# Kernel tuning notes

Measured on AMD Instinct MI355X. Metric: run time of the kernel, lower is better.

Reference implementation:

```python
import jax, jax.numpy as jnp
import numpy as np
from math import comb

# --- module hyperparameters (from init_kwargs / module-level constants) ---
F = 32          # features
NITER = 3       # num_iterations
NB = 16         # num_basis_functions
NDCM = 4        # n_dcm
CUTOFF = 4.0
MAXZ = 17       # max_atomic_number
NC = 9          # (max_degree+1)^2 spherical components, max_degree=2
DEG = np.array([0, 1, 1, 1, 2, 2, 2, 2, 2])  # degree l of each component
BINOM = jnp.asarray([comb(NB - 1, k) for k in range(NB)], dtype=jnp.float32)


def _np_sph9(x, y, z):
    # real spherical harmonics up to l=2 on the unit sphere (numpy, for Gaunt table)
    c0 = 0.28209479177387814; c1 = 0.4886025119029199
    c2a = 1.0925484305920792; c2b = 0.31539156525252005; c2c = 0.5462742152960396
    return np.stack([c0 * np.ones_like(x), c1 * y, c1 * z, c1 * x,
                     c2a * x * y, c2a * y * z, c2b * (3.0 * z * z - 1.0),
                     c2a * x * z, c2c * (x * x - y * y)], axis=0)


def _gaunt():
    # real Gaunt (Clebsch-Gordan-type) coefficients G[a,b,c] = int Y_a Y_b Y_c dOmega
    # via Gauss-Legendre (cos theta) x midpoint (phi) quadrature -- exact for l<=2 products
    ct, wt = np.polynomial.legendre.leggauss(64)
    nph = 256
    phi = (np.arange(nph) + 0.5) * (2.0 * np.pi / nph)
    st = np.sqrt(1.0 - ct ** 2)
    x = st[:, None] * np.cos(phi)[None, :]
    y = st[:, None] * np.sin(phi)[None, :]
    z = np.broadcast_to(ct[:, None], x.shape)
    w = (wt[:, None] * (2.0 * np.pi / nph)) * np.ones((1, nph))
    Y = _np_sph9(x, y, z)
    G = np.einsum('aij,bij,cij,ij->abc', Y, Y, Y, w)
    G[np.abs(G) < 1e-6] = 0.0
    return G

CG = jnp.asarray(_gaunt(), dtype=jnp.float32)  # (9, 9, 9), sparse


def _sph9(u):
    # u: (E, 3) unit vectors -> (E, 9)
    x, y, z = u[:, 0], u[:, 1], u[:, 2]
    c0 = 0.28209479177387814; c1 = 0.4886025119029199
    c2a = 1.0925484305920792; c2b = 0.31539156525252005; c2c = 0.5462742152960396
    return jnp.stack([jnp.full_like(x, c0), c1 * y, c1 * z, c1 * x,
                      c2a * x * y, c2a * y * z, c2b * (3.0 * z * z - 1.0),
                      c2a * x * z, c2c * (x * x - y * y)], axis=-1)


def _radial(r):
    # reciprocal Bernstein radial basis * smooth cutoff; r: (E,) -> (E, NB)
    u = 1.0 / (1.0 + r)
    k = jnp.arange(NB, dtype=jnp.float32)
    rb = BINOM * u[:, None] ** k * (1.0 - u[:, None]) ** (NB - 1 - k)
    t = r / CUTOFF
    den = jnp.where(t < 1.0, 1.0 - t * t, 1.0)
    fc = jnp.where(t < 1.0, jnp.exp(-t * t / den), 0.0)  # smooth_cutoff
    return rb * fc[:, None]


def _equiv_dense(x, W, b=None):
    # per-degree linear (equivariant Dense): x (N, 9, Fin), W (3, Fin, Fout); bias on l=0 only
    y = jnp.einsum('ncf,cfg->ncg', x, W[DEG])
    if b is not None:
        y = y.at[:, 0, :].add(b)
    return y


def _tp(xs, bf):
    # Gaunt tensor-product contraction: out[e,c,f] = sum_ab CG[a,b,c] xs[e,a,f] bf[e,b,f]
    # loop over the 9 fixed output components to avoid an (E,9,9,F) intermediate
    out = []
    for c in range(NC):
        t = jnp.einsum('eaf,ab->ebf', xs, CG[:, :, c])
        out.append(jnp.sum(t * bf, axis=1))
    return jnp.stack(out, axis=1)


def _forward(atomic_numbers, positions, dst_idx, src_idx, embed, Wb, W1, b1, W2, b2,
             Wt00, Wt11, Wmono, element_bias):
    n = atomic_numbers.shape[0]
    disp = positions[src_idx] - positions[dst_idx]                 # (E, 3) gather
    r = jnp.sqrt(jnp.sum(disp * disp, axis=-1) + 1e-12)            # safe norm
    u = disp / r[:, None]
    basis = _sph9(u)[:, :, None] * _radial(r)[:, None, :]          # (E, 9, NB)
    x = jnp.zeros((n, NC, F), dtype=positions.dtype).at[:, 0, :].set(embed[atomic_numbers])
    for i in range(NITER):  # message passing iterations
        bf = jnp.einsum('ebn,bng->ebg', basis, Wb[i][DEG])         # per-degree radial->feature mix (E,9,F)
        msg = _tp(x[src_idx], bf)                                  # gather src + tensor product
        y = x + jax.ops.segment_sum(msg, dst_idx, num_segments=n)  # scatter-aggregate + residual add
        y = _equiv_dense(y, W1[i], b1[i])
        y = jax.nn.silu(y)
        y = _equiv_dense(y, W2[i], b2[i])
        x = x + y                                                  # residual update
    # TensorDense to n_dcm channels, then readout heads
    mono = (x[:, 0, :] @ Wt00) @ Wmono + element_bias[atomic_numbers][:, None]  # (N, NDCM)
    dip = jnp.einsum('ncf,fg->ncg', x[:, 1:4, :], Wt11)            # (N, 3, NDCM) vector channel
    dip = jnp.clip(jax.nn.silu(dip), -0.3, 0.3) + positions[:, :, None]
    return mono, dip


def setup_inputs():
    key = jax.random.key(0)
    ks = jax.random.split(key, 12)
    N, E = 10000, 160000
    return {
        'atomic_numbers': jax.random.randint(ks[0], (N,), 0, MAXZ + 1),
        'positions': jax.random.normal(ks[1], (N, 3), jnp.float32) * 3.0,
        'dst_idx': jax.random.randint(ks[2], (E,), 0, N),
        'src_idx': jax.random.randint(ks[3], (E,), 0, N),
        'embed': jax.random.normal(ks[4], (MAXZ + 1, F), jnp.float32),
        'Wb': jax.random.normal(ks[5], (NITER, 3, NB, F), jnp.float32) / np.sqrt(NB).astype(np.float32),
        'W1': jax.random.normal(ks[6], (NITER, 3, F, F), jnp.float32) / np.sqrt(F).astype(np.float32),
        'b1': jnp.zeros((NITER, F), jnp.float32),
        'W2': jax.random.normal(ks[7], (NITER, 3, F, F), jnp.float32) / np.sqrt(F).astype(np.float32),
        'b2': jnp.zeros((NITER, F), jnp.float32),
        'Wt00': jax.random.normal(ks[8], (F, NDCM), jnp.float32) / np.sqrt(F).astype(np.float32),
        'Wt11': jax.random.normal(ks[9], (F, NDCM), jnp.float32) / np.sqrt(F).astype(np.float32),
        'Wmono': jax.random.normal(ks[10], (NDCM, NDCM), jnp.float32) / np.sqrt(NDCM).astype(np.float32),
        'element_bias': jnp.zeros((MAXZ + 1,), jnp.float32),
    }


def reference(atomic_numbers, positions, dst_idx, src_idx, embed, Wb, W1, b1, W2, b2,
              Wt00, Wt11, Wmono, element_bias):
    return _forward(atomic_numbers, positions, dst_idx, src_idx, embed, Wb, W1, b1, W2, b2,
                    Wt00, Wt11, Wmono, element_bias)
```

## Files before the change

kernel.cpp:

```cpp
#include <hip/hip_runtime.h>
#include <hip/hip_bf16.h>


#define NITER 3
#define BCAP  64

#define OFF_WB    0
#define OFF_W1    4608
#define OFF_B1    13824
#define OFF_W2    13920
#define OFF_B2    23136
#define OFF_WT00  23232
#define OFF_WT11  23360
#define OFF_WMONO 23488
#define OFF_EB    23504
#define OFF_EMB   23522
#define WC_TOTAL  24098

__device__ __forceinline__ float b2f(const __hip_bfloat16 v) { return __bfloat162float(v); }

#define KC0 0.28209479177387814f
#define KG1 0.21850968611841584f
#define KG2 0.12615662610100802f
#define KG3 0.18022375157287861f
#define KG4 0.09011187578643931f
#define KG5 0.15607834722743988f

__device__ __forceinline__ float ldany(const void* p, int i, bool f32) {
    return f32 ? ((const float*)p)[i] : b2f(((const __hip_bfloat16*)p)[i]);
}

__device__ __forceinline__ bool wave_sniff(const void* pos) {
    const __hip_bfloat16* p = (const __hip_bfloat16*)pos;
    int lane = threadIdx.x & 63;
    int bad = 0;
    #pragma unroll
    for (int k = 0; k < 4; k++) {
        float v = b2f(p[lane + k*64]);
        bad |= !(fabsf(v) < 1.0e6f);
    }
    return __ballot(bad) != 0ull;
}

__device__ __forceinline__ float xadd32(float v) {
    return v + __int_as_float(__shfl_xor(__float_as_int(v), 32, 64));
}

__device__ __forceinline__ bool edge_geom(float dx, float dy, float dz,
                                          float* sp, float* rad) {
    float r2 = dx*dx + dy*dy + dz*dz + 1e-12f;
    if (r2 >= 16.0f) return false;
    float r  = sqrtf(r2);
    float t2 = r2 * 0.0625f;
    float fc = __expf(-t2 / (1.0f - t2));
    float u = 1.0f / (1.0f + r);
    float v = 1.0f - u;
    const float BIN[16] = {1.f,15.f,105.f,455.f,1365.f,3003.f,5005.f,6435.f,
                           6435.f,5005.f,3003.f,1365.f,455.f,105.f,15.f,1.f};
    float vp[16];
    vp[0] = 1.0f;
    #pragma unroll
    for (int k = 1; k < 16; k++) vp[k] = vp[k-1] * v;
    float up = 1.0f;
    #pragma unroll
    for (int n = 0; n < 16; n++) { rad[n] = BIN[n] * up * vp[15-n] * fc; up *= u; }
    float ir = 1.0f / r;
    float ux = dx*ir, uy = dy*ir, uz = dz*ir;
    const float c0 = 0.28209479177387814f, c1 = 0.4886025119029199f;
    const float c2a = 1.0925484305920792f, c2b = 0.31539156525252005f, c2c = 0.5462742152960396f;
    sp[0] = c0;
    sp[1] = c1*uy; sp[2] = c1*uz; sp[3] = c1*ux;
    sp[4] = c2a*ux*uy; sp[5] = c2a*uy*uz; sp[6] = c2b*(3.0f*uz*uz - 1.0f);
    sp[7] = c2a*ux*uz; sp[8] = c2c*(ux*ux - uy*uy);
    return true;
}

__global__ void setup_kernel(const void* pos, const void* Wb, const void* W1,
        const void* b1, const void* W2, const void* b2, const void* Wt00,
        const void* Wt11, const void* Wmono, const void* eb, const void* emb,
        const int* __restrict__ an,
        const int* __restrict__ srcI, const int* __restrict__ dstI,
        float* __restrict__ posf, float* __restrict__ wc,
        float* __restrict__ x, float* __restrict__ geo2, int* __restrict__ cur,
        int N, int E, int use_csr) {
    bool f32 = wave_sniff(pos);
    int i = blockIdx.x * blockDim.x + threadIdx.x;
    int np = N * 3;
    if (i < np) { posf[i] = ldany(pos, i, f32); return; }
    int j = i - np;
    if (j < WC_TOTAL) {
        const void* src; int rel;
        if      (j < OFF_W1)    { src = Wb;    rel = j; }
        else if (j < OFF_B1)    { src = W1;    rel = j - OFF_W1; }
        else if (j < OFF_W2)    { src = b1;    rel = j - OFF_B1; }
        else if (j < OFF_B2)    { src = W2;    rel = j - OFF_W2; }
        else if (j < OFF_WT00)  { src = b2;    rel = j - OFF_B2; }
        else if (j < OFF_WT11)  { src = Wt00;  rel = j - OFF_WT00; }
        else if (j < OFF_WMONO) { src = Wt11;  rel = j - OFF_WT11; }
        else if (j < OFF_EB)    { src = Wmono; rel = j - OFF_WMONO; }
        else if (j < OFF_EMB)   { src = eb;    rel = j - OFF_EB; }
        else                    { src = emb;   rel = j - OFF_EMB; }
        wc[j] = ldany(src, rel, f32);
        return;
    }
    j -= WC_TOTAL;
    if (j < N * 32) {
        int n = j >> 5, rem = j & 31;
        x[(size_t)n * 288 + rem] = ldany(emb, an[n] * 32 + rem, f32);
        return;
    }
    j -= N * 32;
    if (j < E && use_csr) {
        int s = srcI[j], d = dstI[j];
        float sp[9], rad[16];
        if (!edge_geom(ldany(pos, s*3+0, f32) - ldany(pos, d*3+0, f32),
                       ldany(pos, s*3+1, f32) - ldany(pos, d*3+1, f32),
                       ldany(pos, s*3+2, f32) - ldany(pos, d*3+2, f32),
                       sp, rad)) return;
        int slot = atomicAdd(&cur[d], 1);
        float* gp = geo2 + ((size_t)d * BCAP + slot) * 32;
        gp[0] = __int_as_float(s);
        gp[1] = 0.0f;
        #pragma unroll
        for (int a = 0; a < 9; a++) gp[2 + a] = sp[a];
        gp[11] = 0.0f;
        #pragma unroll
        for (int k = 0; k < 16; k++) gp[16 + k] = rad[k];
    }
}

template <bool FIRST, bool LAST>
__global__ __launch_bounds__(256) void edge_gather_kernel(
        const float* __restrict__ x, float* __restrict__ y,
        const float* __restrict__ geo2, const int* __restrict__ cur,
        const float* __restrict__ Wbi, int N) {
    int tid  = threadIdx.x;
    int f    = tid & 31;
    int half = (tid >> 5) & 1;
    int n    = (blockIdx.x * blockDim.x + tid) >> 6;
    if (n >= N) return;
    float w0[16], w1[16], w2[16];
    #pragma unroll
    for (int k = 0; k < 16; k++) {
        w0[k] = Wbi[(0*16 + k)*32 + f];
        w1[k] = Wbi[(1*16 + k)*32 + f];
        w2[k] = Wbi[(2*16 + k)*32 + f];
    }
    float A0=0.f,A1=0.f,A2=0.f,A3=0.f,A4=0.f,A5=0.f,A6=0.f,A7=0.f,A8=0.f;
    int beg = n * BCAP, end = beg + cur[n];
    for (int e = beg + half; e < end; e += 2) {
        const float4* gp = (const float4*)(geo2 + (size_t)e * 32);
        float4 h0 = gp[0], h1 = gp[1], h2 = gp[2];
        float4 r0 = gp[4], r1 = gp[5], r2 = gp[6], r3 = gp[7];
        int s = __float_as_int(h0.x);
        float rad[16] = {r0.x,r0.y,r0.z,r0.w, r1.x,r1.y,r1.z,r1.w,
                         r2.x,r2.y,r2.z,r2.w, r3.x,r3.y,r3.z,r3.w};
        float rw0 = 0.f, rw1 = 0.f, rw2 = 0.f;
        #pragma unroll
        for (int k = 0; k < 16; k++) {
            rw0 = fmaf(rad[k], w0[k], rw0);
            rw1 = fmaf(rad[k], w1[k], rw1);
            rw2 = fmaf(rad[k], w2[k], rw2);
        }
        float B0 = h0.z*rw0;
        float B1 = h0.w*rw1, B2 = h1.x*rw1, B3 = h1.y*rw1;
        float B4 = h1.z*rw2, B5 = h1.w*rw2, B6 = h2.x*rw2,
              B7 = h2.y*rw2, B8 = h2.z*rw2;
        const float* xp = x + (size_t)s*288 + f;
        if (FIRST) {
            float X0 = xp[0];
            float k0 = KC0 * X0;
            A0 += k0*B0; A1 += k0*B1; A2 += k0*B2; A3 += k0*B3; A4 += k0*B4;
            A5 += k0*B5; A6 += k0*B6; A7 += k0*B7; A8 += k0*B8;
        } else {
            float X0 = xp[0],   X1 = xp[32],  X2 = xp[64],  X3 = xp[96],  X4 = xp[128];
            float X5 = xp[160], X6 = xp[192], X7 = xp[224], X8 = xp[256];
            A0 += KC0*(X0*B0 + X1*B1 + X2*B2 + X3*B3 + X4*B4 + X5*B5 + X6*B6 + X7*B7 + X8*B8);
            A1 += KC0*(X0*B1 + X1*B0) + KG1*(X3*B4 + X4*B3 + X2*B5 + X5*B2)
                - KG2*(X1*B6 + X6*B1) - KG1*(X1*B8 + X8*B1);
            A2 += KC0*(X0*B2 + X2*B0) + KG1*(X1*B5 + X5*B1 + X3*B7 + X7*B3)
                + 2.0f*KG2*(X2*B6 + X6*B2);
            A3 += KC0*(X0*B3 + X3*B0) + KG1*(X1*B4 + X4*B1 + X2*B7 + X7*B2)
                - KG2*(X3*B6 + X6*B3) + KG1*(X3*B8 + X8*B3);
            if (!LAST) {
                A4 += KC0*(X0*B4 + X4*B0) + KG1*(X1*B3 + X3*B1) + KG5*(X5*B7 + X7*B5)
                    - KG3*(X4*B6 + X6*B4);
                A5 += KC0*(X0*B5 + X5*B0) + KG1*(X1*B2 + X2*B1) + KG5*(X4*B7 + X7*B4)
                    + KG4*(X5*B6 + X6*B5) - KG5*(X5*B8 + X8*B5);
                A6 += KC0*(X0*B6 + X6*B0) - KG2*X1*B1 + 2.0f*KG2*X2*B2 - KG2*X3*B3
                    - KG3*X4*B4 + KG4*X5*B5 + KG3*X6*B6 + KG4*X7*B7 - KG3*X8*B8;
                A7 += KC0*(X0*B7 + X7*B0) + KG1*(X2*B3 + X3*B2) + KG5*(X4*B5 + X5*B4)
                    + KG4*(X6*B7 + X7*B6) + KG5*(X7*B8 + X8*B7);
                A8 += KC0*(X0*B8 + X8*B0) - KG1*X1*B1 + KG1*X3*B3 - KG5*X5*B5 + KG5*X7*B7
                    - KG3*(X6*B8 + X8*B6);
            }
        }
    }
    A0 = xadd32(A0); A1 = xadd32(A1); A2 = xadd32(A2); A3 = xadd32(A3);
    if (!LAST) {
        A4 = xadd32(A4); A5 = xadd32(A5); A6 = xadd32(A6);
        A7 = xadd32(A7); A8 = xadd32(A8);
    }
    if (half == 0) {
        float* yp = y + (size_t)n * 288 + f;
        yp[0]   = A0; yp[32]  = A1; yp[64]  = A2; yp[96]  = A3;
        if (!LAST) {
            yp[128] = A4; yp[160] = A5; yp[192] = A6; yp[224] = A7; yp[256] = A8;
        }
    }
}

template <bool FIRST>
__global__ __launch_bounds__(256) void atom_kernel(
        float* __restrict__ x, const float* __restrict__ y,
        const float* __restrict__ W1i, const float* __restrict__ b1i,
        const float* __restrict__ W2i, const float* __restrict__ b2i,
        int N) {
    __shared__ float sm[4][64*33];
    int lane  = threadIdx.x & 63;
    int wslot = threadIdx.x >> 6;
    int u = __builtin_amdgcn_readfirstlane(blockIdx.x * 4 + wslot);
    int t = u / 9;
    int c = u - t * 9;
    int d = (c == 0) ? 0 : ((c < 4) ? 1 : 2);
    const float* W1 = W1i + d * 1024;
    const float* W2 = W2i + d * 1024;
    float* tile = sm[wslot];
    bool usex = (!FIRST) || (c == 0);
    float4 xr4[8];
    #pragma unroll
    for (int k = 0; k < 8; k++) {
        int e  = lane * 4 + k * 256;
        int al = e >> 5, f = e & 31;
        int ag = t * 64 + al;
        float4 s = make_float4(0.f, 0.f, 0.f, 0.f);
        float4 xv = make_float4(0.f, 0.f, 0.f, 0.f);
        if (ag < N) {
            if (usex) xv = *(const float4*)(x + (size_t)ag * 288 + c * 32 + f);
            float4 yv = *(const float4*)(y + (size_t)ag * 288 + c * 32 + f);
            s = make_float4(xv.x + yv.x, xv.y + yv.y, xv.z + yv.z, xv.w + yv.w);
        }
        xr4[k] = xv;
        *(float4*)(tile + al * 33 + f) = s;
    }
    __syncthreads();
    float yin[32];
    #pragma unroll
    for (int k = 0; k < 8; k++) {
        float4 v = *(const float4*)(tile + lane * 33 + 4 * k);
        yin[4*k+0] = v.x; yin[4*k+1] = v.y; yin[4*k+2] = v.z; yin[4*k+3] = v.w;
    }
    float acc[32];
    #pragma unroll
    for (int g = 0; g < 32; g++) acc[g] = (c == 0) ? b1i[g] : 0.0f;
    #pragma unroll 4
    for (int fi = 0; fi < 32; fi++) {
        float v = yin[fi];
        #pragma unroll
        for (int g = 0; g < 32; g++) acc[g] = fmaf(v, W1[fi*32 + g], acc[g]);
    }
    #pragma unroll
    for (int g = 0; g < 32; g++)
        acc[g] = acc[g] * __builtin_amdgcn_rcpf(1.0f + __expf(-acc[g]));
    float out[32];
    #pragma unroll
    for (int g = 0; g < 32; g++) out[g] = (c == 0) ? b2i[g] : 0.0f;
    #pragma unroll 4
    for (int fi = 0; fi < 32; fi++) {
        float v = acc[fi];
        #pragma unroll
        for (int g = 0; g < 32; g++) out[g] = fmaf(v, W2[fi*32 + g], out[g]);
    }
    __syncthreads();
    #pragma unroll
    for (int k = 0; k < 8; k++)
        *(float4*)(tile + lane * 33 + 4 * k) =
            make_float4(out[4*k+0], out[4*k+1], out[4*k+2], out[4*k+3]);
    __syncthreads();
    #pragma unroll
    for (int k = 0; k < 8; k++) {
        int e  = lane * 4 + k * 256;
        int al = e >> 5, f = e & 31;
        int ag = t * 64 + al;
        if (ag < N) {
            float4 dv = *(const float4*)(tile + al * 33 + f);
            float4 xv = xr4[k];
            *(float4*)(x + (size_t)ag * 288 + c * 32 + f) =
                make_float4(xv.x + dv.x, xv.y + dv.y, xv.z + dv.z, xv.w + dv.w);
        }
    }
}

__global__ __launch_bounds__(256) void atom_readout_kernel(
        const float* __restrict__ x, const float* __restrict__ y,
        const float* __restrict__ W1i, const float* __restrict__ b1i,
        const float* __restrict__ W2i, const float* __restrict__ b2i,
        const int* __restrict__ an, const float* __restrict__ posf,
        const float* __restrict__ wc, const void* __restrict__ pos,
        void* __restrict__ out_, int N) {
    bool f32 = wave_sniff(pos);
    __shared__ float sm[4][64*33];
    int lane  = threadIdx.x & 63;
    int wslot = threadIdx.x >> 6;
    int c = __builtin_amdgcn_readfirstlane(wslot);
    int t = blockIdx.x;
    int d = (c == 0) ? 0 : 1;
    const float* W1 = W1i + d * 1024;
    const float* W2 = W2i + d * 1024;
    float* tile = sm[wslot];
    float4 xr4[8];
    #pragma unroll
    for (int k = 0; k < 8; k++) {
        int e  = lane * 4 + k * 256;
        int al = e >> 5, f = e & 31;
        int ag = t * 64 + al;
        float4 s = make_float4(0.f, 0.f, 0.f, 0.f);
        float4 xv = make_float4(0.f, 0.f, 0.f, 0.f);
        if (ag < N) {
            xv = *(const float4*)(x + (size_t)ag * 288 + c * 32 + f);
            float4 yv = *(const float4*)(y + (size_t)ag * 288 + c * 32 + f);
            s = make_float4(xv.x + yv.x, xv.y + yv.y, xv.z + yv.z, xv.w + yv.w);
        }
        xr4[k] = xv;
        *(float4*)(tile + al * 33 + f) = s;
    }
    __syncthreads();
    float yin[32];
    #pragma unroll
    for (int k = 0; k < 8; k++) {
        float4 v = *(const float4*)(tile + lane * 33 + 4 * k);
        yin[4*k+0] = v.x; yin[4*k+1] = v.y; yin[4*k+2] = v.z; yin[4*k+3] = v.w;
    }
    float acc[32];
    #pragma unroll
    for (int g = 0; g < 32; g++) acc[g] = (c == 0) ? b1i[g] : 0.0f;
    #pragma unroll 4
    for (int fi = 0; fi < 32; fi++) {
        float v = yin[fi];
        #pragma unroll
        for (int g = 0; g < 32; g++) acc[g] = fmaf(v, W1[fi*32 + g], acc[g]);
    }
    #pragma unroll
    for (int g = 0; g < 32; g++)
        acc[g] = acc[g] * __builtin_amdgcn_rcpf(1.0f + __expf(-acc[g]));
    float out[32];
    #pragma unroll
    for (int g = 0; g < 32; g++) out[g] = (c == 0) ? b2i[g] : 0.0f;
    #pragma unroll 4
    for (int fi = 0; fi < 32; fi++) {
        float v = acc[fi];
        #pragma unroll
        for (int g = 0; g < 32; g++) out[g] = fmaf(v, W2[fi*32 + g], out[g]);
    }
    __syncthreads();
    #pragma unroll
    for (int k = 0; k < 8; k++)
        *(float4*)(tile + lane * 33 + 4 * k) =
            make_float4(out[4*k+0], out[4*k+1], out[4*k+2], out[4*k+3]);
    __syncthreads();
    #pragma unroll
    for (int k = 0; k < 8; k++) {
        int e  = lane * 4 + k * 256;
        int al = e >> 5, f = e & 31;
        float4 dv = *(const float4*)(tile + al * 33 + f);
        float4 xv = xr4[k];
        *(float4*)(tile + al * 33 + f) =
            make_float4(xv.x + dv.x, xv.y + dv.y, xv.z + dv.z, xv.w + dv.w);
    }
    __syncthreads();
    if (threadIdx.x < 64) {
        int a  = threadIdx.x;
        int ag = t * 64 + a;
        if (ag < N) {
            const float* Wt00  = wc + OFF_WT00;
            const float* Wt11  = wc + OFF_WT11;
            const float* Wmono = wc + OFF_WMONO;
            const float* x0 = sm[0] + a * 33;
            float q[4] = {0.f, 0.f, 0.f, 0.f};
            for (int f = 0; f < 32; f++) {
                float xv = x0[f];
                #pragma unroll
                for (int j = 0; j < 4; j++) q[j] = fmaf(xv, Wt00[f*4 + j], q[j]);
            }
            float ebv = wc[OFF_EB + an[ag]];
            #pragma unroll
            for (int m = 0; m < 4; m++) {
                float accm = ebv;
                #pragma unroll
                for (int j = 0; j < 4; j++) accm = fmaf(q[j], Wmono[j*4 + m], accm);
                if (f32) ((float*)out_)[ag*4 + m] = accm;
                else ((__hip_bfloat16*)out_)[ag*4 + m] = __float2bfloat16(accm);
            }
            #pragma unroll
            for (int cc = 0; cc < 3; cc++) {
                float pc = posf[ag*3 + cc];
                const float* xc = sm[1 + cc] + a * 33;
                float dq[4] = {0.f, 0.f, 0.f, 0.f};
                for (int f = 0; f < 32; f++) {
                    float xv = xc[f];
                    #pragma unroll
                    for (int m = 0; m < 4; m++) dq[m] = fmaf(xv, Wt11[f*4 + m], dq[m]);
                }
                #pragma unroll
                for (int m = 0; m < 4; m++) {
                    float v = dq[m];
                    v = v * __builtin_amdgcn_rcpf(1.0f + __expf(-v));
                    v = fminf(fmaxf(v, -0.3f), 0.3f);
                    v += pc;
                    if (f32) ((float*)out_)[N*4 + ag*12 + cc*4 + m] = v;
                    else ((__hip_bfloat16*)out_)[N*4 + ag*12 + cc*4 + m] = __float2bfloat16(v);
                }
            }
        }
    }
}

__global__ void zero_kernel(float4* __restrict__ b, int n) {
    int i = blockIdx.x * blockDim.x + threadIdx.x;
    int stride = gridDim.x * blockDim.x;
    float4 z = make_float4(0.f, 0.f, 0.f, 0.f);
    for (; i < n; i += stride) b[i] = z;
}

__global__ __launch_bounds__(256) void edge_inline_kernel(
        const float* __restrict__ x, float* __restrict__ y,
        const float* __restrict__ posf,
        const int* __restrict__ srcI, const int* __restrict__ dstI,
        const float* __restrict__ Wbi, int E) {
    int f  = threadIdx.x & 31;
    int hw = (blockIdx.x * blockDim.x + threadIdx.x) >> 5;
    int nhw = gridDim.x * (blockDim.x >> 5);
    float w0[16], w1[16], w2[16];
    #pragma unroll
    for (int n = 0; n < 16; n++) {
        w0[n] = Wbi[(0*16 + n)*32 + f];
        w1[n] = Wbi[(1*16 + n)*32 + f];
        w2[n] = Wbi[(2*16 + n)*32 + f];
    }
    for (int e = hw; e < E; e += nhw) {
        int s = srcI[e], d = dstI[e];
        float sp[9], rad[16];
        if (!edge_geom(posf[s*3+0] - posf[d*3+0],
                       posf[s*3+1] - posf[d*3+1],
                       posf[s*3+2] - posf[d*3+2], sp, rad)) continue;
        float rw0 = 0.f, rw1 = 0.f, rw2 = 0.f;
        #pragma unroll
        for (int n = 0; n < 16; n++) {
            rw0 = fmaf(rad[n], w0[n], rw0);
            rw1 = fmaf(rad[n], w1[n], rw1);
            rw2 = fmaf(rad[n], w2[n], rw2);
        }
        float B0 = sp[0]*rw0;
        float B1 = sp[1]*rw1, B2 = sp[2]*rw1, B3 = sp[3]*rw1;
        float B4 = sp[4]*rw2, B5 = sp[5]*rw2, B6 = sp[6]*rw2,
              B7 = sp[7]*rw2, B8 = sp[8]*rw2;
        const float* xp = x + (size_t)s*288 + f;
        float X0 = xp[0],   X1 = xp[32],  X2 = xp[64],  X3 = xp[96],  X4 = xp[128];
        float X5 = xp[160], X6 = xp[192], X7 = xp[224], X8 = xp[256];
        float* yp = y + (size_t)d*288 + f;
        float m;
        m = KC0*(X0*B0 + X1*B1 + X2*B2 + X3*B3 + X4*B4 + X5*B5 + X6*B6 + X7*B7 + X8*B8);
        unsafeAtomicAdd(yp + 0, m);
        m = KC0*(X0*B1 + X1*B0) + KG1*(X3*B4 + X4*B3 + X2*B5 + X5*B2)
          - KG2*(X1*B6 + X6*B1) - KG1*(X1*B8 + X8*B1);
        unsafeAtomicAdd(yp + 32, m);
        m = KC0*(X0*B2 + X2*B0) + KG1*(X1*B5 + X5*B1 + X3*B7 + X7*B3)
          + 2.0f*KG2*(X2*B6 + X6*B2);
        unsafeAtomicAdd(yp + 64, m);
        m = KC0*(X0*B3 + X3*B0) + KG1*(X1*B4 + X4*B1 + X2*B7 + X7*B2)
          - KG2*(X3*B6 + X6*B3) + KG1*(X3*B8 + X8*B3);
        unsafeAtomicAdd(yp + 96, m);
        m = KC0*(X0*B4 + X4*B0) + KG1*(X1*B3 + X3*B1) + KG5*(X5*B7 + X7*B5)
          - KG3*(X4*B6 + X6*B4);
        unsafeAtomicAdd(yp + 128, m);
        m = KC0*(X0*B5 + X5*B0) + KG1*(X1*B2 + X2*B1) + KG5*(X4*B7 + X7*B4)
          + KG4*(X5*B6 + X6*B5) - KG5*(X5*B8 + X8*B5);
        unsafeAtomicAdd(yp + 160, m);
        m = KC0*(X0*B6 + X6*B0) - KG2*X1*B1 + 2.0f*KG2*X2*B2 - KG2*X3*B3
          - KG3*X4*B4 + KG4*X5*B5 + KG3*X6*B6 + KG4*X7*B7 - KG3*X8*B8;
        unsafeAtomicAdd(yp + 192, m);
        m = KC0*(X0*B7 + X7*B0) + KG1*(X2*B3 + X3*B2) + KG5*(X4*B5 + X5*B4)
          + KG4*(X6*B7 + X7*B6) + KG5*(X7*B8 + X8*B7);
        unsafeAtomicAdd(yp + 224, m);
        m = KC0*(X0*B8 + X8*B0) - KG1*X1*B1 + KG1*X3*B3 - KG5*X5*B5 + KG5*X7*B7
          - KG3*(X6*B8 + X8*B6);
        unsafeAtomicAdd(yp + 256, m);
    }
}

__global__ void readout_kernel(const float* __restrict__ x,
        const int* __restrict__ an, const float* __restrict__ posf,
        const float* __restrict__ wc, const void* __restrict__ pos,
        void* __restrict__ out, int N) {
    bool f32 = wave_sniff(pos);
    int n = blockIdx.x * blockDim.x + threadIdx.x;
    if (n >= N) return;
    const float* Wt00  = wc + OFF_WT00;
    const float* Wt11  = wc + OFF_WT11;
    const float* Wmono = wc + OFF_WMONO;
    const float* xb = x + (size_t)n * 288;
    float q[4] = {0.f, 0.f, 0.f, 0.f};
    for (int f = 0; f < 32; f++) {
        float xv = xb[f];
        #pragma unroll
        for (int j = 0; j < 4; j++) q[j] = fmaf(xv, Wt00[f*4 + j], q[j]);
    }
    float ebv = wc[OFF_EB + an[n]];
    #pragma unroll
    for (int m = 0; m < 4; m++) {
        float acc = ebv;
        #pragma unroll
        for (int j = 0; j < 4; j++) acc = fmaf(q[j], Wmono[j*4 + m], acc);
        if (f32) ((float*)out)[n*4 + m] = acc;
        else ((__hip_bfloat16*)out)[n*4 + m] = __float2bfloat16(acc);
    }
    #pragma unroll
    for (int c = 0; c < 3; c++) {
        float pc = posf[n*3 + c];
        const float* xc = xb + (1 + c)*32;
        float dq[4] = {0.f, 0.f, 0.f, 0.f};
        for (int f = 0; f < 32; f++) {
            float xv = xc[f];
            #pragma unroll
            for (int m = 0; m < 4; m++) dq[m] = fmaf(xv, Wt11[f*4 + m], dq[m]);
        }
        #pragma unroll
        for (int m = 0; m < 4; m++) {
            float v = dq[m];
            v = v * __builtin_amdgcn_rcpf(1.0f + __expf(-v));
            v = fminf(fmaxf(v, -0.3f), 0.3f);
            v += pc;
            if (f32) ((float*)out)[N*4 + n*12 + c*4 + m] = v;
            else ((__hip_bfloat16*)out)[N*4 + n*12 + c*4 + m] = __float2bfloat16(v);
        }
    }
}

extern "C" void kernel_launch(void* const* d_in, const int* in_sizes, int n_in,
                              void* d_out, int out_size, void* d_ws, size_t ws_size,
                              hipStream_t stream) {
    const int* an    = (const int*)d_in[0];
    const void* pos  = d_in[1];
    const int* dstI  = (const int*)d_in[2];
    const int* srcI  = (const int*)d_in[3];
    const void* embed= d_in[4];
    const void* Wb   = d_in[5];
    const void* W1   = d_in[6];
    const void* b1   = d_in[7];
    const void* W2   = d_in[8];
    const void* b2   = d_in[9];
    const void* Wt00 = d_in[10];
    const void* Wt11 = d_in[11];
    const void* Wmono= d_in[12];
    const void* eb   = d_in[13];
    int N = in_sizes[0];
    int E = in_sizes[2];

    float* x    = (float*)d_ws;
    float* y    = x + (size_t)N * 288;
    float* posf = y + (size_t)N * 288;
    float* wc   = posf + (size_t)N * 3;
    int* cur    = (int*)(wc + WC_TOTAL);
    uintptr_t ga = ((uintptr_t)(cur + N) + 127) & ~(uintptr_t)127;
    float* geo2 = (float*)ga;
    size_t need = (uintptr_t)(geo2 + (size_t)N * BCAP * 32) - (uintptr_t)d_ws;
    bool use_csr = (ws_size >= need);

    hipMemsetAsync(cur, 0, sizeof(int) * (size_t)N, stream);
    if (!use_csr)
        zero_kernel<<<512, 256, 0, stream>>>((float4*)x, N * 72);
    {
        int tot = N * 3 + WC_TOTAL + N * 32 + (use_csr ? E : 0);
        setup_kernel<<<(tot + 255)/256, 256, 0, stream>>>(
            pos, Wb, W1, b1, W2, b2, Wt00, Wt11, Wmono, eb, embed,
            an, srcI, dstI, posf, wc, x, geo2, cur, N, E, use_csr ? 1 : 0);
    }
    int ntiles = (N + 63) / 64;
    if (use_csr) {
        int gblocks = (N + 3) / 4;
        for (int i = 0; i < NITER; i++) {
            const float* Wbi = wc + OFF_WB + (size_t)i*1536;
            const float* W1i = wc + OFF_W1 + (size_t)i*3072;
            const float* b1i = wc + OFF_B1 + (size_t)i*32;
            const float* W2i = wc + OFF_W2 + (size_t)i*3072;
            const float* b2i = wc + OFF_B2 + (size_t)i*32;
            if (i == 0) {
                edge_gather_kernel<true,false><<<gblocks, 256, 0, stream>>>(
                    x, y, geo2, cur, Wbi, N);
                atom_kernel<true><<<(ntiles*9 + 3)/4, 256, 0, stream>>>(
                    x, y, W1i, b1i, W2i, b2i, N);
            } else if (i == NITER - 1) {
                edge_gather_kernel<false,true><<<gblocks, 256, 0, stream>>>(
                    x, y, geo2, cur, Wbi, N);
                atom_readout_kernel<<<ntiles, 256, 0, stream>>>(
                    x, y, W1i, b1i, W2i, b2i, an, posf, wc, pos, d_out, N);
            } else {
                edge_gather_kernel<false,false><<<gblocks, 256, 0, stream>>>(
                    x, y, geo2, cur, Wbi, N);
                atom_kernel<false><<<(ntiles*9 + 3)/4, 256, 0, stream>>>(
                    x, y, W1i, b1i, W2i, b2i, N);
            }
        }
    } else {
        int ablocks = (ntiles * 9 + 3) / 4;
        for (int i = 0; i < NITER; i++) {
            zero_kernel<<<512, 256, 0, stream>>>((float4*)y, N * 72);
            edge_inline_kernel<<<2048, 256, 0, stream>>>(x, y, posf, srcI, dstI,
                wc + OFF_WB + (size_t)i*1536, E);
            atom_kernel<false><<<ablocks, 256, 0, stream>>>(x, y,
                wc + OFF_W1 + (size_t)i*3072, wc + OFF_B1 + (size_t)i*32,
                wc + OFF_W2 + (size_t)i*3072, wc + OFF_B2 + (size_t)i*32, N);
        }
        readout_kernel<<<(N + 255)/256, 256, 0, stream>>>(x, an, posf, wc, pos,
                                                          d_out, N);
    }
}
```

Before: 212.2 us.

## Fuse edge gather and atom update into one kernel per iteration with ping-pong x

Each message-passing iteration now runs as a single kernel per 64-atom tile: it gathers edge messages for the tile's atoms, synchronizes, then runs the atom MLP update, writing to a second x buffer (ping-pong) so other blocks can still read the old features. This removes separate gather/atom launches and the global round trip ordering between them. The tradeoff is far fewer blocks (one per 64 atoms, 4 waves each), so much less parallelism in the gather phase, and the atom phase loops three times with an idle wave. Geometry slot writes are also vectorized to float4 stores.

```diff
diff --git a/kernel.cpp b/kernel.cpp
--- a/kernel.cpp
+++ b/kernel.cpp
@@ -75,70 +75,24 @@
     return true;
 }
 
-__global__ void setup_kernel(const void* pos, const void* Wb, const void* W1,
-        const void* b1, const void* W2, const void* b2, const void* Wt00,
-        const void* Wt11, const void* Wmono, const void* eb, const void* emb,
-        const int* __restrict__ an,
-        const int* __restrict__ srcI, const int* __restrict__ dstI,
-        float* __restrict__ posf, float* __restrict__ wc,
-        float* __restrict__ x, float* __restrict__ geo2, int* __restrict__ cur,
-        int N, int E, int use_csr) {
-    bool f32 = wave_sniff(pos);
-    int i = blockIdx.x * blockDim.x + threadIdx.x;
-    int np = N * 3;
-    if (i < np) { posf[i] = ldany(pos, i, f32); return; }
-    int j = i - np;
-    if (j < WC_TOTAL) {
-        const void* src; int rel;
-        if      (j < OFF_W1)    { src = Wb;    rel = j; }
-        else if (j < OFF_B1)    { src = W1;    rel = j - OFF_W1; }
-        else if (j < OFF_W2)    { src = b1;    rel = j - OFF_B1; }
-        else if (j < OFF_B2)    { src = W2;    rel = j - OFF_W2; }
-        else if (j < OFF_WT00)  { src = b2;    rel = j - OFF_B2; }
-        else if (j < OFF_WT11)  { src = Wt00;  rel = j - OFF_WT00; }
-        else if (j < OFF_WMONO) { src = Wt11;  rel = j - OFF_WT11; }
-        else if (j < OFF_EB)    { src = Wmono; rel = j - OFF_WMONO; }
-        else if (j < OFF_EMB)   { src = eb;    rel = j - OFF_EB; }
-        else                    { src = emb;   rel = j - OFF_EMB; }
-        wc[j] = ldany(src, rel, f32);
-        return;
-    }
-    j -= WC_TOTAL;
-    if (j < N * 32) {
-        int n = j >> 5, rem = j & 31;
-        x[(size_t)n * 288 + rem] = ldany(emb, an[n] * 32 + rem, f32);
-        return;
-    }
-    j -= N * 32;
-    if (j < E && use_csr) {
-        int s = srcI[j], d = dstI[j];
-        float sp[9], rad[16];
-        if (!edge_geom(ldany(pos, s*3+0, f32) - ldany(pos, d*3+0, f32),
-                       ldany(pos, s*3+1, f32) - ldany(pos, d*3+1, f32),
-                       ldany(pos, s*3+2, f32) - ldany(pos, d*3+2, f32),
-                       sp, rad)) return;
-        int slot = atomicAdd(&cur[d], 1);
-        float* gp = geo2 + ((size_t)d * BCAP + slot) * 32;
-        gp[0] = __int_as_float(s);
-        gp[1] = 0.0f;
-        #pragma unroll
-        for (int a = 0; a < 9; a++) gp[2 + a] = sp[a];
-        gp[11] = 0.0f;
-        #pragma unroll
-        for (int k = 0; k < 16; k++) gp[16 + k] = rad[k];
-    }
+__device__ __forceinline__ void write_geo_slot(float* gp, int s,
+                                               const float* sp, const float* rad) {
+    float4* g4 = (float4*)gp;
+    g4[0] = make_float4(__int_as_float(s), 0.f, sp[0], sp[1]);
+    g4[1] = make_float4(sp[2], sp[3], sp[4], sp[5]);
+    g4[2] = make_float4(sp[6], sp[7], sp[8], 0.f);
+    g4[4] = make_float4(rad[0],  rad[1],  rad[2],  rad[3]);
+    g4[5] = make_float4(rad[4],  rad[5],  rad[6],  rad[7]);
+    g4[6] = make_float4(rad[8],  rad[9],  rad[10], rad[11]);
+    g4[7] = make_float4(rad[12], rad[13], rad[14], rad[15]);
 }
 
 template <bool FIRST, bool LAST>
-__global__ __launch_bounds__(256) void edge_gather_kernel(
+__device__ __forceinline__ void gather_phase(
         const float* __restrict__ x, float* __restrict__ y,
         const float* __restrict__ geo2, const int* __restrict__ cur,
-        const float* __restrict__ Wbi, int N) {
-    int tid  = threadIdx.x;
-    int f    = tid & 31;
-    int half = (tid >> 5) & 1;
-    int n    = (blockIdx.x * blockDim.x + tid) >> 6;
-    if (n >= N) return;
+        const float* __restrict__ Wbi, int nend, int f, int half,
+        int wg, int nw) {
     float w0[16], w1[16], w2[16];
     #pragma unroll
     for (int k = 0; k < 16; k++) {
@@ -146,86 +100,82 @@
         w1[k] = Wbi[(1*16 + k)*32 + f];
         w2[k] = Wbi[(2*16 + k)*32 + f];
     }
-    float A0=0.f,A1=0.f,A2=0.f,A3=0.f,A4=0.f,A5=0.f,A6=0.f,A7=0.f,A8=0.f;
-    int beg = n * BCAP, end = beg + cur[n];
-    for (int e = beg + half; e < end; e += 2) {
-        const float4* gp = (const float4*)(geo2 + (size_t)e * 32);
-        float4 h0 = gp[0], h1 = gp[1], h2 = gp[2];
-        float4 r0 = gp[4], r1 = gp[5], r2 = gp[6], r3 = gp[7];
-        int s = __float_as_int(h0.x);
-        float rad[16] = {r0.x,r0.y,r0.z,r0.w, r1.x,r1.y,r1.z,r1.w,
-                         r2.x,r2.y,r2.z,r2.w, r3.x,r3.y,r3.z,r3.w};
-        float rw0 = 0.f, rw1 = 0.f, rw2 = 0.f;
-        #pragma unroll
-        for (int k = 0; k < 16; k++) {
-            rw0 = fmaf(rad[k], w0[k], rw0);
-            rw1 = fmaf(rad[k], w1[k], rw1);
-            rw2 = fmaf(rad[k], w2[k], rw2);
-        }
-        float B0 = h0.z*rw0;
-        float B1 = h0.w*rw1, B2 = h1.x*rw1, B3 = h1.y*rw1;
-        float B4 = h1.z*rw2, B5 = h1.w*rw2, B6 = h2.x*rw2,
-              B7 = h2.y*rw2, B8 = h2.z*rw2;
-        const float* xp = x + (size_t)s*288 + f;
-        if (FIRST) {
-            float X0 = xp[0];
-            float k0 = KC0 * X0;
-            A0 += k0*B0; A1 += k0*B1; A2 += k0*B2; A3 += k0*B3; A4 += k0*B4;
-            A5 += k0*B5; A6 += k0*B6; A7 += k0*B7; A8 += k0*B8;
-        } else {
-            float X0 = xp[0],   X1 = xp[32],  X2 = xp[64],  X3 = xp[96],  X4 = xp[128];
-            float X5 = xp[160], X6 = xp[192], X7 = xp[224], X8 = xp[256];
-            A0 += KC0*(X0*B0 + X1*B1 + X2*B2 + X3*B3 + X4*B4 + X5*B5 + X6*B6 + X7*B7 + X8*B8);
-            A1 += KC0*(X0*B1 + X1*B0) + KG1*(X3*B4 + X4*B3 + X2*B5 + X5*B2)
-                - KG2*(X1*B6 + X6*B1) - KG1*(X1*B8 + X8*B1);
-            A2 += KC0*(X0*B2 + X2*B0) + KG1*(X1*B5 + X5*B1 + X3*B7 + X7*B3)
-                + 2.0f*KG2*(X2*B6 + X6*B2);
-            A3 += KC0*(X0*B3 + X3*B0) + KG1*(X1*B4 + X4*B1 + X2*B7 + X7*B2)
-                - KG2*(X3*B6 + X6*B3) + KG1*(X3*B8 + X8*B3);
+    for (int n = wg; n < nend; n += nw) {
+        float A0=0.f,A1=0.f,A2=0.f,A3=0.f,A4=0.f,A5=0.f,A6=0.f,A7=0.f,A8=0.f;
+        int beg = n * BCAP, end = beg + cur[n];
+        for (int e = beg + half; e < end; e += 2) {
+            const float4* gp = (const float4*)(geo2 + (size_t)e * 32);
+            float4 h0 = gp[0], h1 = gp[1], h2 = gp[2];
+            float4 r0 = gp[4], r1 = gp[5], r2 = gp[6], r3 = gp[7];
+            int s = __float_as_int(h0.x);
+            float rad[16] = {r0.x,r0.y,r0.z,r0.w, r1.x,r1.y,r1.z,r1.w,
+                             r2.x,r2.y,r2.z,r2.w, r3.x,r3.y,r3.z,r3.w};
+            float rw0 = 0.f, rw1 = 0.f, rw2 = 0.f;
+            #pragma unroll
+            for (int k = 0; k < 16; k++) {
+                rw0 = fmaf(rad[k], w0[k], rw0);
+                rw1 = fmaf(rad[k], w1[k], rw1);
+                rw2 = fmaf(rad[k], w2[k], rw2);
+            }
+            float B0 = h0.z*rw0;
+            float B1 = h0.w*rw1, B2 = h1.x*rw1, B3 = h1.y*rw1;
+            float B4 = h1.z*rw2, B5 = h1.w*rw2, B6 = h2.x*rw2,
+                  B7 = h2.y*rw2, B8 = h2.z*rw2;
+            const float* xp = x + (size_t)s*288 + f;
+            if (FIRST) {
+                float X0 = xp[0];
+                float k0 = KC0 * X0;
+                A0 += k0*B0; A1 += k0*B1; A2 += k0*B2; A3 += k0*B3; A4 += k0*B4;
+                A5 += k0*B5; A6 += k0*B6; A7 += k0*B7; A8 += k0*B8;
+            } else {
+                float X0 = xp[0],   X1 = xp[32],  X2 = xp[64],  X3 = xp[96],  X4 = xp[128];
+                float X5 = xp[160], X6 = xp[192], X7 = xp[224], X8 = xp[256];
+                A0 += KC0*(X0*B0 + X1*B1 + X2*B2 + X3*B3 + X4*B4 + X5*B5 + X6*B6 + X7*B7 + X8*B8);
+                A1 += KC0*(X0*B1 + X1*B0) + KG1*(X3*B4 + X4*B3 + X2*B5 + X5*B2)
+                    - KG2*(X1*B6 + X6*B1) - KG1*(X1*B8 + X8*B1);
+                A2 += KC0*(X0*B2 + X2*B0) + KG1*(X1*B5 + X5*B1 + X3*B7 + X7*B3)
+                    + 2.0f*KG2*(X2*B6 + X6*B2);
+                A3 += KC0*(X0*B3 + X3*B0) + KG1*(X1*B4 + X4*B1 + X2*B7 + X7*B2)
+                    - KG2*(X3*B6 + X6*B3) + KG1*(X3*B8 + X8*B3);
+                if (!LAST) {
+                    A4 += KC0*(X0*B4 + X4*B0) + KG1*(X1*B3 + X3*B1) + KG5*(X5*B7 + X7*B5)
+                        - KG3*(X4*B6 + X6*B4);
+                    A5 += KC0*(X0*B5 + X5*B0) + KG1*(X1*B2 + X2*B1) + KG5*(X4*B7 + X7*B4)
+                        + KG4*(X5*B6 + X6*B5) - KG5*(X5*B8 + X8*B5);
+                    A6 += KC0*(X0*B6 + X6*B0) - KG2*X1*B1 + 2.0f*KG2*X2*B2 - KG2*X3*B3
+                        - KG3*X4*B4 + KG4*X5*B5 + KG3*X6*B6 + KG4*X7*B7 - KG3*X8*B8;
+                    A7 += KC0*(X0*B7 + X7*B0) + KG1*(X2*B3 + X3*B2) + KG5*(X4*B5 + X5*B4)
+                        + KG4*(X6*B7 + X7*B6) + KG5*(X7*B8 + X8*B7);
+                    A8 += KC0*(X0*B8 + X8*B0) - KG1*X1*B1 + KG1*X3*B3 - KG5*X5*B5 + KG5*X7*B7
+                        - KG3*(X6*B8 + X8*B6);
+                }
+            }
+        }
+        A0 = xadd32(A0); A1 = xadd32(A1); A2 = xadd32(A2); A3 = xadd32(A3);
+        if (!LAST) {
+            A4 = xadd32(A4); A5 = xadd32(A5); A6 = xadd32(A6);
+            A7 = xadd32(A7); A8 = xadd32(A8);
+        }
+        if (half == 0) {
+            float* yp = y + (size_t)n * 288 + f;
+            yp[0]   = A0; yp[32]  = A1; yp[64]  = A2; yp[96]  = A3;
             if (!LAST) {
-                A4 += KC0*(X0*B4 + X4*B0) + KG1*(X1*B3 + X3*B1) + KG5*(X5*B7 + X7*B5)
-                    - KG3*(X4*B6 + X6*B4);
-                A5 += KC0*(X0*B5 + X5*B0) + KG1*(X1*B2 + X2*B1) + KG5*(X4*B7 + X7*B4)
-                    + KG4*(X5*B6 + X6*B5) - KG5*(X5*B8 + X8*B5);
-                A6 += KC0*(X0*B6 + X6*B0) - KG2*X1*B1 + 2.0f*KG2*X2*B2 - KG2*X3*B3
-                    - KG3*X4*B4 + KG4*X5*B5 + KG3*X6*B6 + KG4*X7*B7 - KG3*X8*B8;
-                A7 += KC0*(X0*B7 + X7*B0) + KG1*(X2*B3 + X3*B2) + KG5*(X4*B5 + X5*B4)
-                    + KG4*(X6*B7 + X7*B6) + KG5*(X7*B8 + X8*B7);
-                A8 += KC0*(X0*B8 + X8*B0) - KG1*X1*B1 + KG1*X3*B3 - KG5*X5*B5 + KG5*X7*B7
-                    - KG3*(X6*B8 + X8*B6);
+                yp[128] = A4; yp[160] = A5; yp[192] = A6; yp[224] = A7; yp[256] = A8;
             }
         }
     }
-    A0 = xadd32(A0); A1 = xadd32(A1); A2 = xadd32(A2); A3 = xadd32(A3);
-    if (!LAST) {
-        A4 = xadd32(A4); A5 = xadd32(A5); A6 = xadd32(A6);
-        A7 = xadd32(A7); A8 = xadd32(A8);
-    }
-    if (half == 0) {
-        float* yp = y + (size_t)n * 288 + f;
-        yp[0]   = A0; yp[32]  = A1; yp[64]  = A2; yp[96]  = A3;
-        if (!LAST) {
-            yp[128] = A4; yp[160] = A5; yp[192] = A6; yp[224] = A7; yp[256] = A8;
-        }
-    }
 }
 
 template <bool FIRST>
-__global__ __launch_bounds__(256) void atom_kernel(
-        float* __restrict__ x, const float* __restrict__ y,
+__device__ __forceinline__ void atom_unit(
+        const float* __restrict__ xin, float* __restrict__ xout,
+        const float* __restrict__ y,
         const float* __restrict__ W1i, const float* __restrict__ b1i,
         const float* __restrict__ W2i, const float* __restrict__ b2i,
-        int N) {
-    __shared__ float sm[4][64*33];
-    int lane  = threadIdx.x & 63;
-    int wslot = threadIdx.x >> 6;
-    int u = __builtin_amdgcn_readfirstlane(blockIdx.x * 4 + wslot);
-    int t = u / 9;
-    int c = u - t * 9;
+        int N, int t, int c, int lane, float* __restrict__ tile) {
     int d = (c == 0) ? 0 : ((c < 4) ? 1 : 2);
     const float* W1 = W1i + d * 1024;
     const float* W2 = W2i + d * 1024;
-    float* tile = sm[wslot];
     bool usex = (!FIRST) || (c == 0);
     float4 xr4[8];
     #pragma unroll
@@ -236,7 +186,7 @@
         float4 s = make_float4(0.f, 0.f, 0.f, 0.f);
         float4 xv = make_float4(0.f, 0.f, 0.f, 0.f);
         if (ag < N) {
-            if (usex) xv = *(const float4*)(x + (size_t)ag * 288 + c * 32 + f);
+            if (usex) xv = *(const float4*)(xin + (size_t)ag * 288 + c * 32 + f);
             float4 yv = *(const float4*)(y + (size_t)ag * 288 + c * 32 + f);
             s = make_float4(xv.x + yv.x, xv.y + yv.y, xv.z + yv.z, xv.w + yv.w);
         }
@@ -285,25 +235,22 @@
         if (ag < N) {
             float4 dv = *(const float4*)(tile + al * 33 + f);
             float4 xv = xr4[k];
-            *(float4*)(x + (size_t)ag * 288 + c * 32 + f) =
+            *(float4*)(xout + (size_t)ag * 288 + c * 32 + f) =
                 make_float4(xv.x + dv.x, xv.y + dv.y, xv.z + dv.z, xv.w + dv.w);
         }
     }
 }
 
-__global__ __launch_bounds__(256) void atom_readout_kernel(
+__device__ __forceinline__ void atom_readout_unit(
         const float* __restrict__ x, const float* __restrict__ y,
         const float* __restrict__ W1i, const float* __restrict__ b1i,
         const float* __restrict__ W2i, const float* __restrict__ b2i,
         const int* __restrict__ an, const float* __restrict__ posf,
-        const float* __restrict__ wc, const void* __restrict__ pos,
-        void* __restrict__ out_, int N) {
-    bool f32 = wave_sniff(pos);
-    __shared__ float sm[4][64*33];
+        const float* __restrict__ wc, bool f32, void* __restrict__ out_,
+        int N, int t, float sm[4][2112]) {
     int lane  = threadIdx.x & 63;
     int wslot = threadIdx.x >> 6;
     int c = __builtin_amdgcn_readfirstlane(wslot);
-    int t = blockIdx.x;
     int d = (c == 0) ? 0 : 1;
     const float* W1 = W1i + d * 1024;
     const float* W2 = W2i + d * 1024;
@@ -415,6 +362,147 @@
     }
 }
 
+template <bool FIRST>
+__global__ __launch_bounds__(256) void fused_iter_kernel(
+        const float* __restrict__ xin, float* __restrict__ xout,
+        float* __restrict__ y,
+        const float* __restrict__ geo2, const int* __restrict__ cur,
+        const float* __restrict__ Wbi,
+        const float* __restrict__ W1i, const float* __restrict__ b1i,
+        const float* __restrict__ W2i, const float* __restrict__ b2i, int N) {
+    __shared__ float sm[4][64*33];
+    int tid   = threadIdx.x;
+    int lane  = tid & 63;
+    int wslot = tid >> 6;
+    int f     = tid & 31;
+    int half  = (tid >> 5) & 1;
+    int t     = blockIdx.x;
+    int nend  = (N < (t + 1) * 64) ? N : (t + 1) * 64;
+    gather_phase<FIRST, false>(xin, y, geo2, cur, Wbi, nend, f, half,
+                               t * 64 + wslot, 4);
+    __syncthreads();
+    #pragma unroll 1
+    for (int r = 0; r < 3; r++) {
+        int c = wslot + r * 4;
+        int tt = (c < 9) ? t : (1 << 20);
+        int cc = (c < 9) ? c : 0;
+        atom_unit<FIRST>(xin, xout, y, W1i, b1i, W2i, b2i, N, tt, cc,
+                         lane, sm[wslot]);
+    }
+}
+
+__global__ __launch_bounds__(256) void fused_last_kernel(
+        const float* __restrict__ xin, float* __restrict__ y,
+        const float* __restrict__ geo2, const int* __restrict__ cur,
+        const float* __restrict__ Wbi,
+        const float* __restrict__ W1i, const float* __restrict__ b1i,
+        const float* __restrict__ W2i, const float* __restrict__ b2i,
+        const int* __restrict__ an, const float* __restrict__ posf,
+        const float* __restrict__ wc, const void* __restrict__ pos,
+        void* __restrict__ out_, int N) {
+    bool f32 = wave_sniff(pos);
+    __shared__ float sm[4][64*33];
+    int tid   = threadIdx.x;
+    int f     = tid & 31;
+    int half  = (tid >> 5) & 1;
+    int wslot = tid >> 6;
+    int t     = blockIdx.x;
+    int nend  = (N < (t + 1) * 64) ? N : (t + 1) * 64;
+    gather_phase<false, true>(xin, y, geo2, cur, Wbi, nend, f, half,
+                              t * 64 + wslot, 4);
+    __syncthreads();
+    atom_readout_unit(xin, y, W1i, b1i, W2i, b2i, an, posf, wc, f32, out_,
+                      N, t, sm);
+}
+
+
+__global__ void setup_kernel(const void* pos, const void* Wb, const void* W1,
+        const void* b1, const void* W2, const void* b2, const void* Wt00,
+        const void* Wt11, const void* Wmono, const void* eb, const void* emb,
+        const int* __restrict__ an,
+        const int* __restrict__ srcI, const int* __restrict__ dstI,
+        float* __restrict__ posf, float* __restrict__ wc,
+        float* __restrict__ x, float* __restrict__ geo2, int* __restrict__ cur,
+        int N, int E, int use_csr) {
+    bool f32 = wave_sniff(pos);
+    int i = blockIdx.x * blockDim.x + threadIdx.x;
+    int np = N * 3;
+    if (i < np) { posf[i] = ldany(pos, i, f32); return; }
+    int j = i - np;
+    if (j < WC_TOTAL) {
+        const void* src; int rel;
+        if      (j < OFF_W1)    { src = Wb;    rel = j; }
+        else if (j < OFF_B1)    { src = W1;    rel = j - OFF_W1; }
+        else if (j < OFF_W2)    { src = b1;    rel = j - OFF_B1; }
+        else if (j < OFF_B2)    { src = W2;    rel = j - OFF_W2; }
+        else if (j < OFF_WT00)  { src = b2;    rel = j - OFF_B2; }
+        else if (j < OFF_WT11)  { src = Wt00;  rel = j - OFF_WT00; }
+        else if (j < OFF_WMONO) { src = Wt11;  rel = j - OFF_WT11; }
+        else if (j < OFF_EB)    { src = Wmono; rel = j - OFF_WMONO; }
+        else if (j < OFF_EMB)   { src = eb;    rel = j - OFF_EB; }
+        else                    { src = emb;   rel = j - OFF_EMB; }
+        wc[j] = ldany(src, rel, f32);
+        return;
+    }
+    j -= WC_TOTAL;
+    if (j < N * 32) {
+        int n = j >> 5, rem = j & 31;
+        x[(size_t)n * 288 + rem] = ldany(emb, an[n] * 32 + rem, f32);
+        return;
+    }
+    j -= N * 32;
+    if (j < E && use_csr) {
+        int s = srcI[j], d = dstI[j];
+        float sp[9], rad[16];
+        if (!edge_geom(ldany(pos, s*3+0, f32) - ldany(pos, d*3+0, f32),
+                       ldany(pos, s*3+1, f32) - ldany(pos, d*3+1, f32),
+                       ldany(pos, s*3+2, f32) - ldany(pos, d*3+2, f32),
+                       sp, rad)) return;
+        int slot = atomicAdd(&cur[d], 1);
+        write_geo_slot(geo2 + ((size_t)d * BCAP + slot) * 32, s, sp, rad);
+    }
+}
+
+template <bool FIRST, bool LAST>
+__global__ __launch_bounds__(256) void edge_gather_kernel(
+        const float* __restrict__ x, float* __restrict__ y,
+        const float* __restrict__ geo2, const int* __restrict__ cur,
+        const float* __restrict__ Wbi, int N) {
+    int tid  = threadIdx.x;
+    int f    = tid & 31;
+    int half = (tid >> 5) & 1;
+    int wg   = (blockIdx.x * blockDim.x + tid) >> 6;
+    gather_phase<FIRST, LAST>(x, y, geo2, cur, Wbi, N, f, half, wg, N);
+}
+
+template <bool FIRST>
+__global__ __launch_bounds__(256) void atom_kernel(
+        float* __restrict__ x, const float* __restrict__ y,
+        const float* __restrict__ W1i, const float* __restrict__ b1i,
+        const float* __restrict__ W2i, const float* __restrict__ b2i,
+        int N) {
+    __shared__ float sm[4][64*33];
+    int lane  = threadIdx.x & 63;
+    int wslot = threadIdx.x >> 6;
+    int u = __builtin_amdgcn_readfirstlane(blockIdx.x * 4 + wslot);
+    int t = u / 9;
+    int c = u - t * 9;
+    atom_unit<FIRST>(x, x, y, W1i, b1i, W2i, b2i, N, t, c, lane, sm[wslot]);
+}
+
+__global__ __launch_bounds__(256) void atom_readout_kernel(
+        const float* __restrict__ x, const float* __restrict__ y,
+        const float* __restrict__ W1i, const float* __restrict__ b1i,
+        const float* __restrict__ W2i, const float* __restrict__ b2i,
+        const int* __restrict__ an, const float* __restrict__ posf,
+        const float* __restrict__ wc, const void* __restrict__ pos,
+        void* __restrict__ out_, int N) {
+    bool f32 = wave_sniff(pos);
+    __shared__ float sm[4][64*33];
+    atom_readout_unit(x, y, W1i, b1i, W2i, b2i, an, posf, wc, f32, out_,
+                      N, blockIdx.x, sm);
+}
+
 __global__ void zero_kernel(float4* __restrict__ b, int n) {
     int i = blockIdx.x * blockDim.x + threadIdx.x;
     int stride = gridDim.x * blockDim.x;
@@ -555,6 +643,39 @@
     const void* eb   = d_in[13];
     int N = in_sizes[0];
     int E = in_sizes[2];
+    int ntiles = (N + 63) / 64;
+
+    {
+        float* x0   = (float*)d_ws;
+        float* x1   = x0 + (size_t)N * 288;
+        float* y    = x1 + (size_t)N * 288;
+        float* posf = y + (size_t)N * 288;
+        float* wc   = posf + (size_t)N * 3;
+        int* cur    = (int*)(wc + WC_TOTAL);
+        uintptr_t ga = ((uintptr_t)(cur + N) + 127) & ~(uintptr_t)127;
+        float* geo2 = (float*)ga;
+        size_t need = (uintptr_t)(geo2 + (size_t)N * BCAP * 32) - (uintptr_t)d_ws;
+        if (ws_size >= need) {
+            hipMemsetAsync(cur, 0, sizeof(int) * (size_t)N, stream);
+            int tot = N * 3 + WC_TOTAL + N * 32 + E;
+            setup_kernel<<<(tot + 255)/256, 256, 0, stream>>>(
+                pos, Wb, W1, b1, W2, b2, Wt00, Wt11, Wmono, eb, embed,
+                an, srcI, dstI, posf, wc, x0, geo2, cur, N, E, 1);
+            fused_iter_kernel<true><<<ntiles, 256, 0, stream>>>(
+                x0, x1, y, geo2, cur,
+                wc + OFF_WB, wc + OFF_W1, wc + OFF_B1, wc + OFF_W2, wc + OFF_B2, N);
+            fused_iter_kernel<false><<<ntiles, 256, 0, stream>>>(
+                x1, x0, y, geo2, cur,
+                wc + OFF_WB + 1536, wc + OFF_W1 + 3072, wc + OFF_B1 + 32,
+                wc + OFF_W2 + 3072, wc + OFF_B2 + 32, N);
+            fused_last_kernel<<<ntiles, 256, 0, stream>>>(
+                x0, y, geo2, cur,
+                wc + OFF_WB + 3072, wc + OFF_W1 + 6144, wc + OFF_B1 + 64,
+                wc + OFF_W2 + 6144, wc + OFF_B2 + 64,
+                an, posf, wc, pos, d_out, N);
+            return;
+        }
+    }
 
     float* x    = (float*)d_ws;
     float* y    = x + (size_t)N * 288;
@@ -575,7 +696,6 @@
             pos, Wb, W1, b1, W2, b2, Wt00, Wt11, Wmono, eb, embed,
             an, srcI, dstI, posf, wc, x, geo2, cur, N, E, use_csr ? 1 : 0);
     }
-    int ntiles = (N + 63) / 64;
     if (use_csr) {
         int gblocks = (N + 3) / 4;
         for (int i = 0; i < NITER; i++) {
```

New measurement: 372.7 us. +75.6%, slower.
